# Kernel tuning notes

Hardware: AMD Instinct MI355X
Metric: run time of the kernel (lower is better)

## Reference

```python
import jax, jax.numpy as jnp
import numpy as np

B, S, QS, KS, F, H = 4, 2048, 512, 1024, 1024, 16
DH = F // H  # head dim = 64


def setup_inputs() -> dict:
    key = jax.random.key(0)
    ks = jax.random.split(key, 7)
    s = 0.02
    return {
        "x": jax.random.normal(ks[0], (B, S, QS), dtype=jnp.float32),
        "y": jax.random.normal(ks[1], (B, S, QS), dtype=jnp.float32),
        "z": jax.random.normal(ks[2], (B, S, KS), dtype=jnp.float32),
        "Wq": jax.random.normal(ks[3], (2 * QS, F), dtype=jnp.float32) * s,
        "Wk": jax.random.normal(ks[4], (KS, F), dtype=jnp.float32) * s,
        "Wv": jax.random.normal(ks[5], (KS, F), dtype=jnp.float32) * s,
        "Wo": jax.random.normal(ks[6], (F, F), dtype=jnp.float32) * s,
    }


def _split_heads(t):
    # [B, S, F] -> [B, H, S, DH]
    return t.reshape(B, S, H, DH).transpose(0, 2, 1, 3)


def reference(x, y, z, Wq, Wk, Wv, Wo):
    q = _split_heads(jnp.concatenate([x, y], axis=-1) @ Wq)  # [B,H,S,DH]
    k = _split_heads(z @ Wk)
    v = _split_heads(z @ Wv)
    scale = 1.0 / jnp.sqrt(jnp.asarray(DH, dtype=q.dtype))
    scores = jnp.einsum("bhsd,bhtd->bhst", q, k) * scale  # [B,H,S,S]
    attn = jax.nn.softmax(scores, axis=-1)
    out = jnp.einsum("bhst,bhtd->bhsd", attn, v)  # [B,H,S,DH]
    out = out.transpose(0, 2, 1, 3).reshape(B, S, F)
    return out @ Wo
```

## Files before the change

### kernel.cpp

```cpp
#include <hip/hip_runtime.h>

typedef __attribute__((ext_vector_type(8))) short short8;
typedef __attribute__((ext_vector_type(4))) float f32x4;
typedef __attribute__((ext_vector_type(16))) float f32x16;
typedef __attribute__((ext_vector_type(4))) unsigned short us4;
typedef __attribute__((ext_vector_type(4))) unsigned int u32x4;

#define GLOAD16(gsrc, ldst)                                             \
  __builtin_amdgcn_global_load_lds(                                     \
      (const __attribute__((address_space(1))) unsigned int*)(gsrc),    \
      (__attribute__((address_space(3))) unsigned int*)(ldst), 16, 0, 0)

#define VMEM_DRAIN_BARRIER()                              \
  do {                                                    \
    asm volatile("s_waitcnt vmcnt(0)" ::: "memory");      \
    __builtin_amdgcn_sched_barrier(0);                    \
    __syncthreads();                                      \
  } while (0)

#if __has_builtin(__builtin_amdgcn_exp2f)
#define EXP2F(x) __builtin_amdgcn_exp2f(x)
#else
#define EXP2F(x) exp2f(x)
#endif

static __device__ __forceinline__ unsigned short f2bf(float f) {
  unsigned int u = __float_as_uint(f);
  u += 0x7fffu + ((u >> 16) & 1u);
  return (unsigned short)(u >> 16);
}

static __device__ __forceinline__ unsigned cvtpk(float lo, float hi) {
  unsigned r;
  asm("v_cvt_pk_bf16_f32 %0, %1, %2" : "=v"(r) : "v"(lo), "v"(hi));
  return r;
}

__global__ __launch_bounds__(256) void prep(const float* __restrict__ x,
                                            const float* __restrict__ y,
                                            const float* __restrict__ z,
                                            const float* __restrict__ Wq,
                                            const float* __restrict__ Wk,
                                            const float* __restrict__ Wv,
                                            const float* __restrict__ Wo,
                                            unsigned short* __restrict__ XY,
                                            unsigned short* __restrict__ Z,
                                            unsigned short* __restrict__ WqT,
                                            unsigned short* __restrict__ WkT,
                                            unsigned short* __restrict__ WvT,
                                            unsigned short* __restrict__ WoT) {
  __shared__ __align__(16) unsigned short LT[64 * 72];
  const int bid = blockIdx.x, t = threadIdx.x;

  if (bid < 2048) {
    const int NX = (8192 * 512) / 4;
    const int NZ = (8192 * 1024) / 4;
    const int total = 2 * NX + NZ;
    for (int idx = bid * 256 + t; idx < total; idx += 2048 * 256) {
      const float* src;
      unsigned short* dst;
      if (idx < NX) {
        int p = idx * 4; int row = p >> 9, c = p & 511;
        src = x + p; dst = XY + (size_t)row * 1024 + c;
      } else if (idx < 2 * NX) {
        int p = (idx - NX) * 4; int row = p >> 9, c = p & 511;
        src = y + p; dst = XY + (size_t)row * 1024 + 512 + c;
      } else {
        int p = (idx - 2 * NX) * 4;
        src = z + p; dst = Z + p;
      }
      float4 v = *(const float4*)src;
      us4 o; o[0] = f2bf(v.x); o[1] = f2bf(v.y); o[2] = f2bf(v.z); o[3] = f2bf(v.w);
      *(us4*)dst = o;
    }
    return;
  }

  const int seg = (bid - 2048) >> 8;
  const int local = (bid - 2048) & 255;
  const float* W = (seg == 0) ? Wq : (seg == 1) ? Wk : (seg == 2) ? Wv : Wo;
  unsigned short* WT = (seg == 0) ? WqT : (seg == 1) ? WkT : (seg == 2) ? WvT : WoT;
  const int k0 = (local >> 4) * 64, n0 = (local & 15) * 64;
#pragma unroll
  for (int j = 0; j < 4; ++j) {
    int r = j * 16 + (t >> 4);
    int c = (t & 15) * 4;
    float4 w = *(const float4*)(W + (size_t)(k0 + r) * 1024 + n0 + c);
    LT[(c + 0) * 72 + r] = f2bf(w.x);
    LT[(c + 1) * 72 + r] = f2bf(w.y);
    LT[(c + 2) * 72 + r] = f2bf(w.z);
    LT[(c + 3) * 72 + r] = f2bf(w.w);
  }
  __syncthreads();
#pragma unroll
  for (int j = 0; j < 2; ++j) {
    int n = j * 32 + (t >> 3), ch = t & 7;
    *(short8*)(WT + (size_t)(n0 + n) * 1024 + k0 + ch * 8) =
        *(const short8*)(LT + n * 72 + ch * 8);
  }
}

__global__ __launch_bounds__(256) void qkv_gemm(const unsigned short* __restrict__ XY,
                                                const unsigned short* __restrict__ Zb,
                                                const unsigned short* __restrict__ WqT,
                                                const unsigned short* __restrict__ WkT,
                                                const unsigned short* __restrict__ WvT,
                                                unsigned short* __restrict__ Qb,
                                                unsigned short* __restrict__ Kb,
                                                unsigned short* __restrict__ Vtg) {
  __shared__ __align__(16) unsigned short As[128 * 64];
  __shared__ __align__(16) unsigned short Bs[128 * 64];
  const int tid = threadIdx.x;
  const int lane = tid & 63, wid = tid >> 6;
  const int lq = lane & 15, lg = lane >> 4;
  const int wr = wid >> 1, wc = wid & 1;
  const int seg = blockIdx.x >> 3;
  const int m0 = blockIdx.y * 128, n0 = (blockIdx.x & 7) * 128;

  const unsigned short* A;
  const unsigned short* Bt;
  float scale;
  if (seg == 0)      { A = XY; Bt = WqT; scale = 0.18033688011112042f; }
  else if (seg == 1) { A = Zb; Bt = WkT; scale = 1.0f; }
  else               { A = Zb; Bt = WvT; scale = 1.0f; }

  const int srr = tid >> 3;
  const int gg = (tid & 7) ^ (srr & 7);

  f32x4 acc[4][4] = {};

  for (int k0 = 0; k0 < 1024; k0 += 64) {
    __syncthreads();
#pragma unroll
    for (int i = 0; i < 4; ++i) {
      int r = i * 32 + srr;
      GLOAD16(A + (size_t)(m0 + r) * 1024 + k0 + gg * 8,
              (char*)As + i * 4096 + wid * 1024);
      GLOAD16(Bt + (size_t)(n0 + r) * 1024 + k0 + gg * 8,
              (char*)Bs + i * 4096 + wid * 1024);
    }
    VMEM_DRAIN_BARRIER();
#pragma unroll
    for (int kk = 0; kk < 2; ++kk) {
      short8 af[4], bfr[4];
#pragma unroll
      for (int mf = 0; mf < 4; ++mf) {
        int r = wr * 64 + mf * 16 + lq;
        int c = (kk * 4 + lg) ^ (r & 7);
        af[mf] = *(const short8*)(As + r * 64 + c * 8);
      }
#pragma unroll
      for (int nf = 0; nf < 4; ++nf) {
        int r = wc * 64 + nf * 16 + lq;
        int c = (kk * 4 + lg) ^ (r & 7);
        bfr[nf] = *(const short8*)(Bs + r * 64 + c * 8);
      }
#pragma unroll
      for (int mf = 0; mf < 4; ++mf)
#pragma unroll
        for (int nf = 0; nf < 4; ++nf)
          acc[mf][nf] = __builtin_amdgcn_mfma_f32_16x16x32_bf16(af[mf], bfr[nf],
                                                                acc[mf][nf], 0, 0, 0);
    }
  }

  if (seg == 2) {
    const int bq = m0 >> 11;
    const int sbase = (m0 & 2047) + wr * 64;
#pragma unroll
    for (int mf = 0; mf < 4; ++mf)
#pragma unroll
      for (int nf = 0; nf < 4; ++nf) {
        int col = n0 + wc * 64 + nf * 16 + lq;
        int hh = col >> 6, dd = col & 63;
        int s = sbase + mf * 16 + lg * 4;
        us4 o4;
#pragma unroll
        for (int j = 0; j < 4; ++j) o4[j] = f2bf(acc[mf][nf][j]);
        *(us4*)(Vtg + ((size_t)(bq * 16 + hh) * 64 + dd) * 2048 + s) = o4;
      }
  } else {
    unsigned short* C = (seg == 0) ? Qb : Kb;
#pragma unroll
    for (int mf = 0; mf < 4; ++mf)
#pragma unroll
      for (int nf = 0; nf < 4; ++nf)
#pragma unroll
        for (int j = 0; j < 4; ++j) {
          int row = m0 + wr * 64 + mf * 16 + lg * 4 + j;
          int col = n0 + wc * 64 + nf * 16 + lq;
          C[(size_t)row * 1024 + col] = f2bf(acc[mf][nf][j] * scale);
        }
  }
}

__global__ __launch_bounds__(256) void gemm_nt(const unsigned short* __restrict__ A,
                                               const unsigned short* __restrict__ Bt,
                                               float* __restrict__ Cout) {
  __shared__ __align__(16) unsigned short As[128 * 64];
  __shared__ __align__(16) unsigned short Bs[128 * 64];
  const int tid = threadIdx.x;
  const int lane = tid & 63, wid = tid >> 6;
  const int lq = lane & 15, lg = lane >> 4;
  const int wr = wid >> 1, wc = wid & 1;
  const int m0 = blockIdx.y * 128, n0 = blockIdx.x * 128;

  const int srr = tid >> 3;
  const int gg = (tid & 7) ^ (srr & 7);

  f32x4 acc[4][4] = {};

  for (int k0 = 0; k0 < 1024; k0 += 64) {
    __syncthreads();
#pragma unroll
    for (int i = 0; i < 4; ++i) {
      int r = i * 32 + srr;
      GLOAD16(A + (size_t)(m0 + r) * 1024 + k0 + gg * 8,
              (char*)As + i * 4096 + wid * 1024);
      GLOAD16(Bt + (size_t)(n0 + r) * 1024 + k0 + gg * 8,
              (char*)Bs + i * 4096 + wid * 1024);
    }
    VMEM_DRAIN_BARRIER();
#pragma unroll
    for (int kk = 0; kk < 2; ++kk) {
      short8 af[4], bfr[4];
#pragma unroll
      for (int mf = 0; mf < 4; ++mf) {
        int r = wr * 64 + mf * 16 + lq;
        int c = (kk * 4 + lg) ^ (r & 7);
        af[mf] = *(const short8*)(As + r * 64 + c * 8);
      }
#pragma unroll
      for (int nf = 0; nf < 4; ++nf) {
        int r = wc * 64 + nf * 16 + lq;
        int c = (kk * 4 + lg) ^ (r & 7);
        bfr[nf] = *(const short8*)(Bs + r * 64 + c * 8);
      }
#pragma unroll
      for (int mf = 0; mf < 4; ++mf)
#pragma unroll
        for (int nf = 0; nf < 4; ++nf)
          acc[mf][nf] = __builtin_amdgcn_mfma_f32_16x16x32_bf16(af[mf], bfr[nf],
                                                                acc[mf][nf], 0, 0, 0);
    }
  }

#pragma unroll
  for (int mf = 0; mf < 4; ++mf)
#pragma unroll
    for (int nf = 0; nf < 4; ++nf)
#pragma unroll
      for (int j = 0; j < 4; ++j) {
        int row = m0 + wr * 64 + mf * 16 + lg * 4 + j;
        int col = n0 + wc * 64 + nf * 16 + lq;
        Cout[(size_t)row * 1024 + col] = acc[mf][nf][j];
      }
}

__global__ __launch_bounds__(512, 4) void attn8(const unsigned short* __restrict__ Q,
                                                const unsigned short* __restrict__ K,
                                                const unsigned short* __restrict__ Vt,
                                                unsigned short* __restrict__ AO) {
  __shared__ __align__(16) unsigned short Ks[2][64 * 64];
  __shared__ __align__(16) unsigned short Vs[2][64 * 64];

  const int lin = blockIdx.x + (blockIdx.y << 3);
  const int xcd = lin & 7, rest = lin >> 3;
  const int bh = xcd * 8 + (rest >> 3);
  const int q0 = (rest & 7) * 256;
  const int b = bh >> 4, h = bh & 15;

  const int tid = threadIdx.x, lane = tid & 63, w = tid >> 6;
  const int l31 = lane & 31, hi = lane >> 5;
  const int swz = l31 & 7;

  short8 qf[4];
#pragma unroll
  for (int dblk = 0; dblk < 4; ++dblk)
    qf[dblk] = *(const short8*)(Q + (size_t)(b * 2048 + q0 + w * 32 + l31) * 1024 +
                                h * 64 + dblk * 16 + hi * 8);

  short8 ones;
#pragma unroll
  for (int e = 0; e < 8; ++e) ones[e] = (short)0x3F80;

#define STAGE(bf, t)                                                               \
  do {                                                                             \
    {                                                                              \
      int r = tid >> 3, c = tid & 7, g = c ^ (r & 7);                              \
      GLOAD16(K + (size_t)(b * 2048 + (t) * 64 + r) * 1024 + h * 64 + g * 8,       \
              (char*)Ks[bf] + w * 1024);                                           \
      GLOAD16(Vt + ((size_t)bh * 64 + r) * 2048 + (t) * 64 + g * 8,                \
              (char*)Vs[bf] + w * 1024);                                           \
    }                                                                              \
  } while (0)

  STAGE(0, 0);
  VMEM_DRAIN_BARRIER();

  f32x16 od[2] = {};
  f32x16 sums = {};
  int buf = 0;

  for (int t = 0; t < 32; ++t) {
    if (t < 31) STAGE(buf ^ 1, t + 1);

    f32x16 st[2];
    __builtin_amdgcn_s_setprio(1);
#pragma unroll
    for (int kh = 0; kh < 2; ++kh) {
      f32x16 a = {};
#pragma unroll
      for (int dblk = 0; dblk < 4; ++dblk) {
        short8 kf = *(const short8*)(Ks[buf] + (kh * 32 + l31) * 64 +
                                     (((dblk * 2 + hi) ^ swz) * 8));
        a = __builtin_amdgcn_mfma_f32_32x32x16_bf16(kf, qf[dblk], a, 0, 0, 0);
      }
      st[kh] = a;
    }
    __builtin_amdgcn_s_setprio(0);

#pragma unroll
    for (int kh = 0; kh < 2; ++kh)
#pragma unroll
      for (int r = 0; r < 16; ++r) st[kh][r] = EXP2F(st[kh][r]);

    __builtin_amdgcn_s_setprio(1);
#pragma unroll
    for (int ks = 0; ks < 4; ++ks) {
      const int tt = ks >> 1, cm = (ks & 1) * 2;
      unsigned a_lo = cvtpk(st[tt][cm * 4 + 0], st[tt][cm * 4 + 1]);
      unsigned a_hi = cvtpk(st[tt][cm * 4 + 2], st[tt][cm * 4 + 3]);
      unsigned b_lo = cvtpk(st[tt][cm * 4 + 4], st[tt][cm * 4 + 5]);
      unsigned b_hi = cvtpk(st[tt][cm * 4 + 6], st[tt][cm * 4 + 7]);
      auto Xlo = __builtin_amdgcn_permlane32_swap(a_lo, b_lo, false, false);
      auto Xhi = __builtin_amdgcn_permlane32_swap(a_hi, b_hi, false, false);
      u32x4 up;
      up[0] = Xlo[0];
      up[1] = Xhi[0];
      up[2] = Xlo[1];
      up[3] = Xhi[1];
      short8 pa = __builtin_bit_cast(short8, up);
      sums = __builtin_amdgcn_mfma_f32_32x32x16_bf16(ones, pa, sums, 0, 0, 0);
#pragma unroll
      for (int td = 0; td < 2; ++td) {
        short8 vf = *(const short8*)(Vs[buf] + (td * 32 + l31) * 64 +
                                     (((ks * 2 + hi) ^ swz) * 8));
        od[td] = __builtin_amdgcn_mfma_f32_32x32x16_bf16(vf, pa, od[td], 0, 0, 0);
      }
    }
    __builtin_amdgcn_s_setprio(0);

    VMEM_DRAIN_BARRIER();
    buf ^= 1;
  }

  float inv = 1.0f / sums[0];
  const size_t orow = (size_t)(b * 2048 + q0 + w * 32 + l31);
#pragma unroll
  for (int td = 0; td < 2; ++td)
#pragma unroll
    for (int rh = 0; rh < 4; ++rh) {
      us4 o4;
#pragma unroll
      for (int rl = 0; rl < 4; ++rl) o4[rl] = f2bf(od[td][rh * 4 + rl] * inv);
      *(us4*)(AO + orow * 1024 + h * 64 + td * 32 + rh * 8 + hi * 4) = o4;
    }
#undef STAGE
}

extern "C" void kernel_launch(void* const* d_in, const int* in_sizes, int n_in,
                              void* d_out, int out_size, void* d_ws, size_t ws_size,
                              hipStream_t stream) {
  const float* x = (const float*)d_in[0];
  const float* y = (const float*)d_in[1];
  const float* z = (const float*)d_in[2];
  const float* Wq = (const float*)d_in[3];
  const float* Wk = (const float*)d_in[4];
  const float* Wv = (const float*)d_in[5];
  const float* Wo = (const float*)d_in[6];

  char* ws = (char*)d_ws;
  unsigned short* XY  = (unsigned short*)(ws + 0);
  unsigned short* Zb  = (unsigned short*)(ws + 16777216);
  unsigned short* WqT = (unsigned short*)(ws + 33554432);
  unsigned short* WkT = (unsigned short*)(ws + 35651584);
  unsigned short* WvT = (unsigned short*)(ws + 37748736);
  unsigned short* WoT = (unsigned short*)(ws + 39845888);
  unsigned short* Qb  = (unsigned short*)(ws + 41943040);
  unsigned short* Kb  = (unsigned short*)(ws + 58720256);
  unsigned short* Vtg = (unsigned short*)(ws + 92274688);
  unsigned short* AO  = (unsigned short*)(ws + 109051904);

  prep<<<3072, 256, 0, stream>>>(x, y, z, Wq, Wk, Wv, Wo,
                                 XY, Zb, WqT, WkT, WvT, WoT);

  qkv_gemm<<<dim3(24, 64), 256, 0, stream>>>(XY, Zb, WqT, WkT, WvT, Qb, Kb, Vtg);

  attn8<<<dim3(8, 64), 512, 0, stream>>>(Qb, Kb, Vtg, AO);

  gemm_nt<<<dim3(8, 64), 256, 0, stream>>>(AO, WoT, (float*)d_out);
}
```

Measured before the change: 195.8 us.

## Rewrite QKV GEMM as 256x256 tile, 8-wave double-buffered pipelined kernel

Replaces the 128x128, 4-wave QKV projection GEMM with a 256x256 tile kernel using 8 waves and double-buffered LDS. Global-to-LDS loads for the next K-tiles are issued between MFMA phases, and the waits are staggered with vmcnt counters and barriers, so memory traffic overlaps with compute. s_setprio is raised around the MFMA clusters. The larger tile improves operand reuse but uses 128KB of LDS at one block per CU and launches only 384 blocks, which may underfill the device. The fine-grained barrier choreography also risks races if the wait counts are off.

```diff
diff --git a/kernel.cpp b/kernel.cpp
--- a/kernel.cpp
+++ b/kernel.cpp
@@ -10,6 +10,11 @@
   __builtin_amdgcn_global_load_lds(                                     \
       (const __attribute__((address_space(1))) unsigned int*)(gsrc),    \
       (__attribute__((address_space(3))) unsigned int*)(ldst), 16, 0, 0)
+
+#define SB() __builtin_amdgcn_sched_barrier(0)
+#define BAR() __builtin_amdgcn_s_barrier()
+#define WAITV(N) asm volatile("s_waitcnt vmcnt(" #N ")" ::: "memory")
+#define WAITL0() asm volatile("s_waitcnt lgkmcnt(0)" ::: "memory")
 
 #define VMEM_DRAIN_BARRIER()                              \
   do {                                                    \
@@ -100,22 +105,20 @@
   }
 }
 
-__global__ __launch_bounds__(256) void qkv_gemm(const unsigned short* __restrict__ XY,
-                                                const unsigned short* __restrict__ Zb,
-                                                const unsigned short* __restrict__ WqT,
-                                                const unsigned short* __restrict__ WkT,
-                                                const unsigned short* __restrict__ WvT,
-                                                unsigned short* __restrict__ Qb,
-                                                unsigned short* __restrict__ Kb,
-                                                unsigned short* __restrict__ Vtg) {
-  __shared__ __align__(16) unsigned short As[128 * 64];
-  __shared__ __align__(16) unsigned short Bs[128 * 64];
+__global__ __launch_bounds__(512, 1) void qkv_gemm8(
+    const unsigned short* __restrict__ XY, const unsigned short* __restrict__ Zb,
+    const unsigned short* __restrict__ WqT, const unsigned short* __restrict__ WkT,
+    const unsigned short* __restrict__ WvT, unsigned short* __restrict__ Qb,
+    unsigned short* __restrict__ Kb, unsigned short* __restrict__ Vtg) {
+  __shared__ __align__(16) unsigned short As_[2][2][128 * 64];
+  __shared__ __align__(16) unsigned short Bs_[2][2][128 * 64];
+
   const int tid = threadIdx.x;
-  const int lane = tid & 63, wid = tid >> 6;
+  const int lane = tid & 63, w = tid >> 6;
   const int lq = lane & 15, lg = lane >> 4;
-  const int wr = wid >> 1, wc = wid & 1;
-  const int seg = blockIdx.x >> 3;
-  const int m0 = blockIdx.y * 128, n0 = (blockIdx.x & 7) * 128;
+  const int wr = w >> 2, wc = w & 3;
+  const int seg = blockIdx.x >> 2;
+  const int n0 = (blockIdx.x & 3) * 256, m0 = blockIdx.y * 256;
 
   const unsigned short* A;
   const unsigned short* Bt;
@@ -124,56 +127,130 @@
   else if (seg == 1) { A = Zb; Bt = WkT; scale = 1.0f; }
   else               { A = Zb; Bt = WvT; scale = 1.0f; }
 
-  const int srr = tid >> 3;
-  const int gg = (tid & 7) ^ (srr & 7);
-
-  f32x4 acc[4][4] = {};
-
-  for (int k0 = 0; k0 < 1024; k0 += 64) {
-    __syncthreads();
-#pragma unroll
-    for (int i = 0; i < 4; ++i) {
-      int r = i * 32 + srr;
-      GLOAD16(A + (size_t)(m0 + r) * 1024 + k0 + gg * 8,
-              (char*)As + i * 4096 + wid * 1024);
-      GLOAD16(Bt + (size_t)(n0 + r) * 1024 + k0 + gg * 8,
-              (char*)Bs + i * 4096 + wid * 1024);
-    }
-    VMEM_DRAIN_BARRIER();
-#pragma unroll
-    for (int kk = 0; kk < 2; ++kk) {
-      short8 af[4], bfr[4];
-#pragma unroll
-      for (int mf = 0; mf < 4; ++mf) {
-        int r = wr * 64 + mf * 16 + lq;
-        int c = (kk * 4 + lg) ^ (r & 7);
-        af[mf] = *(const short8*)(As + r * 64 + c * 8);
-      }
-#pragma unroll
-      for (int nf = 0; nf < 4; ++nf) {
-        int r = wc * 64 + nf * 16 + lq;
-        int c = (kk * 4 + lg) ^ (r & 7);
-        bfr[nf] = *(const short8*)(Bs + r * 64 + c * 8);
-      }
-#pragma unroll
-      for (int mf = 0; mf < 4; ++mf)
-#pragma unroll
-        for (int nf = 0; nf < 4; ++nf)
-          acc[mf][nf] = __builtin_amdgcn_mfma_f32_16x16x32_bf16(af[mf], bfr[nf],
-                                                                acc[mf][nf], 0, 0, 0);
-    }
-  }
+  const int sr_ = tid >> 3;
+  const int gg_ = (tid & 7) ^ (sr_ & 7);
+
+#define STAGE_A(kt1, h)                                                       \
+  do { int b_ = (kt1) & 1, kk_ = ((kt1) & 15) * 64;                           \
+    _Pragma("unroll")                                                         \
+    for (int i = 0; i < 2; ++i) {                                             \
+      int r_ = i * 64 + sr_;                                                  \
+      GLOAD16(A + (size_t)(m0 + (h) * 128 + r_) * 1024 + kk_ + gg_ * 8,       \
+              (char*)As_[b_][h] + i * 8192 + w * 1024);                       \
+    } } while (0)
+
+#define STAGE_B(kt1, h)                                                       \
+  do { int b_ = (kt1) & 1, kk_ = ((kt1) & 15) * 64;                           \
+    _Pragma("unroll")                                                         \
+    for (int i = 0; i < 2; ++i) {                                             \
+      int r_ = i * 64 + sr_;                                                  \
+      GLOAD16(Bt + (size_t)(n0 + (h) * 128 + r_) * 1024 + kk_ + gg_ * 8,      \
+              (char*)Bs_[b_][h] + i * 8192 + w * 1024);                       \
+    } } while (0)
+
+  f32x4 acc[8][4] = {};
+
+  STAGE_A(0, 0); STAGE_A(0, 1); STAGE_B(0, 0); STAGE_B(0, 1);
+  STAGE_B(1, 0); STAGE_B(1, 1);
+  WAITV(4); SB();
+  __syncthreads();
+
+#pragma unroll 2
+  for (int kt = 0; kt < 16; ++kt) {
+    const int cb = kt & 1;
+    const unsigned short* Ac = As_[cb][wr];
+    const unsigned short* Bc = Bs_[cb][wc >> 1];
+    const int brow = (wc & 1) * 64;
+
+    short8 bfr0[4], bfr1[4], af[4];
+
+#pragma unroll
+    for (int nf = 0; nf < 4; ++nf) {
+      int r = brow + nf * 16 + lq;
+      bfr0[nf] = *(const short8*)(Bc + r * 64 + ((lg ^ (r & 7)) * 8));
+      bfr1[nf] = *(const short8*)(Bc + r * 64 + (((4 + lg) ^ (r & 7)) * 8));
+    }
+#pragma unroll
+    for (int mf = 0; mf < 4; ++mf) {
+      int r = mf * 16 + lq;
+      af[mf] = *(const short8*)(Ac + r * 64 + ((lg ^ (r & 7)) * 8));
+    }
+    STAGE_A(kt + 1, 0);
+    SB(); BAR(); WAITL0(); SB();
+    __builtin_amdgcn_s_setprio(1);
+#pragma unroll
+    for (int mf = 0; mf < 4; ++mf)
+#pragma unroll
+      for (int nf = 0; nf < 4; ++nf)
+        acc[mf][nf] = __builtin_amdgcn_mfma_f32_16x16x32_bf16(af[mf], bfr0[nf],
+                                                              acc[mf][nf], 0, 0, 0);
+    __builtin_amdgcn_s_setprio(0);
+    SB(); BAR(); SB();
+
+#pragma unroll
+    for (int mf = 0; mf < 4; ++mf) {
+      int r = 64 + mf * 16 + lq;
+      af[mf] = *(const short8*)(Ac + r * 64 + ((lg ^ (r & 7)) * 8));
+    }
+    STAGE_A(kt + 1, 1);
+    SB(); BAR(); WAITL0(); SB();
+    __builtin_amdgcn_s_setprio(1);
+#pragma unroll
+    for (int mf = 0; mf < 4; ++mf)
+#pragma unroll
+      for (int nf = 0; nf < 4; ++nf)
+        acc[4 + mf][nf] = __builtin_amdgcn_mfma_f32_16x16x32_bf16(af[mf], bfr0[nf],
+                                                                  acc[4 + mf][nf], 0, 0, 0);
+    __builtin_amdgcn_s_setprio(0);
+    SB(); BAR(); SB();
+
+#pragma unroll
+    for (int mf = 0; mf < 4; ++mf) {
+      int r = mf * 16 + lq;
+      af[mf] = *(const short8*)(Ac + r * 64 + (((4 + lg) ^ (r & 7)) * 8));
+    }
+    STAGE_B(kt + 2, 0);
+    SB(); BAR(); WAITL0(); SB();
+    __builtin_amdgcn_s_setprio(1);
+#pragma unroll
+    for (int mf = 0; mf < 4; ++mf)
+#pragma unroll
+      for (int nf = 0; nf < 4; ++nf)
+        acc[mf][nf] = __builtin_amdgcn_mfma_f32_16x16x32_bf16(af[mf], bfr1[nf],
+                                                              acc[mf][nf], 0, 0, 0);
+    __builtin_amdgcn_s_setprio(0);
+    SB(); BAR(); SB();
+
+#pragma unroll
+    for (int mf = 0; mf < 4; ++mf) {
+      int r = 64 + mf * 16 + lq;
+      af[mf] = *(const short8*)(Ac + r * 64 + (((4 + lg) ^ (r & 7)) * 8));
+    }
+    STAGE_B(kt + 2, 1);
+    SB(); BAR(); WAITL0(); SB();
+    __builtin_amdgcn_s_setprio(1);
+#pragma unroll
+    for (int mf = 0; mf < 4; ++mf)
+#pragma unroll
+      for (int nf = 0; nf < 4; ++nf)
+        acc[4 + mf][nf] = __builtin_amdgcn_mfma_f32_16x16x32_bf16(af[mf], bfr1[nf],
+                                                                  acc[4 + mf][nf], 0, 0, 0);
+    __builtin_amdgcn_s_setprio(0);
+    WAITV(4); SB(); BAR(); SB();
+  }
+#undef STAGE_A
+#undef STAGE_B
 
   if (seg == 2) {
     const int bq = m0 >> 11;
-    const int sbase = (m0 & 2047) + wr * 64;
-#pragma unroll
-    for (int mf = 0; mf < 4; ++mf)
+#pragma unroll
+    for (int mf = 0; mf < 8; ++mf)
 #pragma unroll
       for (int nf = 0; nf < 4; ++nf) {
         int col = n0 + wc * 64 + nf * 16 + lq;
         int hh = col >> 6, dd = col & 63;
-        int s = sbase + mf * 16 + lg * 4;
+        int row = m0 + wr * 128 + mf * 16 + lg * 4;
+        int s = row & 2047;
         us4 o4;
 #pragma unroll
         for (int j = 0; j < 4; ++j) o4[j] = f2bf(acc[mf][nf][j]);
@@ -182,12 +259,12 @@
   } else {
     unsigned short* C = (seg == 0) ? Qb : Kb;
 #pragma unroll
-    for (int mf = 0; mf < 4; ++mf)
+    for (int mf = 0; mf < 8; ++mf)
 #pragma unroll
       for (int nf = 0; nf < 4; ++nf)
 #pragma unroll
         for (int j = 0; j < 4; ++j) {
-          int row = m0 + wr * 64 + mf * 16 + lg * 4 + j;
+          int row = m0 + wr * 128 + mf * 16 + lg * 4 + j;
           int col = n0 + wc * 64 + nf * 16 + lq;
           C[(size_t)row * 1024 + col] = f2bf(acc[mf][nf][j] * scale);
         }
@@ -395,7 +472,7 @@
   prep<<<3072, 256, 0, stream>>>(x, y, z, Wq, Wk, Wv, Wo,
                                  XY, Zb, WqT, WkT, WvT, WoT);
 
-  qkv_gemm<<<dim3(24, 64), 256, 0, stream>>>(XY, Zb, WqT, WkT, WvT, Qb, Kb, Vtg);
+  qkv_gemm8<<<dim3(12, 32), 512, 0, stream>>>(XY, Zb, WqT, WkT, WvT, Qb, Kb, Vtg);
 
   attn8<<<dim3(8, 64), 512, 0, stream>>>(Qb, Kb, Vtg, AO);
 
```

Measured after the change: 215.9 us. 10.2% more time.
